# Kernel tuning notes

Hardware: AMD Instinct MI355X
Metric: run time of the kernel (lower is better)

The kernel has to match this reference:

```python
import jax, jax.numpy as jnp
import numpy as np


def _layernorm(x, g, b, eps=1e-5):
    mu = jnp.mean(x, axis=-1, keepdims=True)
    var = jnp.var(x, axis=-1, keepdims=True)
    return (x - mu) * jax.lax.rsqrt(var + eps) * g + b


def _forward(x_real, x_imag, dt, conv_w, conv_b, spec_re, spec_im, lam_re, lam_im,
             dt_param, sigma, noise_r, noise_i, ln_g, ln_b, W1, b1, w2, b2,
             Jg_W, Jg_b, Rg_W, Rg_b):
    B, T, C, H, W = x_real.shape
    x = x_real + 1j * x_imag  # complex field [B,T,C,H,W]

    # ---- spatial mixer: 3x3 conv applied to real/imag parts (linear op) ----
    def conv(z):
        z2 = z.reshape(B * T, C, H, W)
        y = jax.lax.conv_general_dilated(z2, conv_w, (1, 1), 'SAME',
                                         dimension_numbers=('NCHW', 'OIHW', 'NCHW'))
        return (y + conv_b[None, :, None, None]).reshape(B, T, C, H, W)
    x = x + (conv(x.real) + 1j * conv(x.imag))

    # ---- spectral mixer: pointwise complex filter in FFT domain ----
    Xf = jnp.fft.fft2(x, axes=(-2, -1), norm='ortho')
    filt = (spec_re + 1j * spec_im)[None, None]  # [1,1,C,H,W]
    x = x + jnp.fft.ifft2(Xf * filt, axes=(-2, -1), norm='ortho')

    # ---- metriplectic propagator: diagonal SSM scan in rfft2 space ----
    dt_eff = dt * jax.nn.softplus(dt_param)          # [C]
    dt_scalar = dt_eff.mean()
    xs = jnp.concatenate([x.real, x.imag], axis=0)   # [2B,T,C,H,W]; B_out=2B
    u = jnp.fft.rfft2(xs, axes=(-2, -1), norm='ortho')  # [2B,T,C,H,Wf]
    lam = -jax.nn.softplus(lam_re) + 1j * lam_im     # stable poles, [C]
    A = jnp.exp(lam * dt_eff.astype(jnp.complex64))  # [C]
    A = jnp.broadcast_to(A[None, None, :, None, None], u.shape)

    def comb(e1, e2):  # first-order linear recurrence h_t = a_t h_{t-1} + u_t
        a1, u1 = e1
        a2, u2 = e2
        return (a1 * a2, a2 * u1 + u2)
    _, h = jax.lax.associative_scan(comb, (A, u), axis=1)

    xt = jnp.fft.irfft2(h, s=(H, W), axes=(-2, -1), norm='ortho')  # [2B,T,C,H,W] real
    x_temporal = xt[:B] + 1j * xt[B:]

    noise = (noise_r + 1j * noise_i) * sigma * jnp.sqrt(dt_scalar)
    x = x + x_temporal + noise

    # ---- Port-Hamiltonian layer on real||imag channel concat ----
    xp = jnp.transpose(x, (0, 1, 3, 4, 2))                  # [B,T,H,W,C]
    xc = jnp.concatenate([xp.real, xp.imag], axis=-1)       # [B,T,H,W,2C]
    D = 2 * C
    x_in = _layernorm(xc, ln_g, ln_b)
    # grads of potential H = sum(MLP(x_in)) wrt x_in
    pot = lambda z: (jax.nn.silu(z @ W1 + b1) @ w2 + b2).sum()
    grads = jax.grad(pot)(x_in)
    M = (x_in @ Jg_W + Jg_b).reshape(*xc.shape[:-1], D, D)
    Jm = M - jnp.swapaxes(M, -1, -2)
    P = (x_in @ Rg_W + Rg_b).reshape(*xc.shape[:-1], D, D)
    R = jnp.einsum('...ki,...kj->...ij', P, P) + 1e-4 * jnp.eye(D, dtype=xc.dtype)
    update = jnp.einsum('...ij,...j->...i', Jm - R, grads)
    x_ph = xc + update * dt_scalar

    # output: [B,T,2C,H,W]; real half = out.real, imag half = out.imag
    return jnp.transpose(x_ph, (0, 1, 4, 2, 3))


def setup_inputs() -> dict:
    key = jax.random.key(0)
    ks = jax.random.split(key, 16)
    B, T, C, H, W = 2, 8, 16, 64, 64
    D = 2 * C
    hid = D * 4
    f32 = jnp.float32
    rn = lambda k, s, sc=1.0: jax.random.normal(k, s, f32) * sc
    return dict(
        x_real=rn(ks[0], (B, T, C, H, W)),
        x_imag=rn(ks[1], (B, T, C, H, W)),
        dt=jnp.asarray(0.1, f32),
        conv_w=rn(ks[2], (C, C, 3, 3), 0.05),
        conv_b=jnp.zeros((C,), f32),
        spec_re=rn(ks[3], (C, H, W), 0.1),
        spec_im=rn(ks[4], (C, H, W), 0.1),
        lam_re=rn(ks[5], (C,)),
        lam_im=rn(ks[6], (C,)),
        dt_param=rn(ks[7], (C,)),
        sigma=jnp.asarray(0.01, f32),
        noise_r=rn(ks[8], (B, T, C, H, W)),
        noise_i=rn(ks[9], (B, T, C, H, W)),
        ln_g=jnp.ones((D,), f32),
        ln_b=jnp.zeros((D,), f32),
        W1=rn(ks[10], (D, hid), 0.1),
        b1=jnp.zeros((hid,), f32),
        w2=rn(ks[11], (hid,), 0.1),
        b2=jnp.asarray(0.0, f32),
        Jg_W=rn(ks[12], (D, D * D), 0.02),
        Jg_b=jnp.zeros((D * D,), f32),
        Rg_W=rn(ks[13], (D, D * D), 0.02),
        Rg_b=jnp.zeros((D * D,), f32),
    )


def reference(x_real, x_imag, dt, conv_w, conv_b, spec_re, spec_im, lam_re, lam_im,
              dt_param, sigma, noise_r, noise_i, ln_g, ln_b, W1, b1, w2, b2,
              Jg_W, Jg_b, Rg_W, Rg_b):
    return _forward(x_real, x_imag, dt, conv_w, conv_b, spec_re, spec_im, lam_re,
                    lam_im, dt_param, sigma, noise_r, noise_i, ln_g, ln_b, W1, b1,
                    w2, b2, Jg_W, Jg_b, Rg_W, Rg_b)
```

## Files before the change

kernel.cpp:

```cpp
#include <hip/hip_runtime.h>
#include <math.h>
#include <utility>

#define Bb 2
#define Tt 8
#define Cc 16
#define Hh 64
#define Ww 64
#define Dd 32
#define HID 128
#define NPIX 4096
#define NIMG 256

typedef unsigned short ushort_t;
typedef unsigned int uint_t;
typedef __attribute__((ext_vector_type(8))) short short8;
typedef __attribute__((ext_vector_type(4))) float f32x4;
union U16 { uint4 u; short8 s; };

__device__ __forceinline__ float sp_f(float x) {
    return (x > 20.f) ? x : log1pf(expf(x));
}

__device__ __forceinline__ ushort_t f2bf(float f) {
    uint_t u = __float_as_uint(f);
    uint_t r = (u + 0x7fffu + ((u >> 16) & 1u)) >> 16;
    return (ushort_t)r;
}
__device__ __forceinline__ float bf2f(ushort_t h) { return __uint_as_float(((uint_t)h) << 16); }

__device__ __forceinline__ uint_t packbf(float hi, float lo) {
    return __builtin_amdgcn_perm(__float_as_uint(hi), __float_as_uint(lo), 0x07060302u);
}
__device__ __forceinline__ uint4 synth8(const float* gf, float xs) {
    uint4 r;
    r.x = packbf(gf[1] * xs, gf[0] * xs);
    r.y = packbf(gf[3] * xs, gf[2] * xs);
    r.z = packbf(gf[5] * xs, gf[4] * xs);
    r.w = packbf(gf[7] * xs, gf[6] * xs);
    return r;
}
__device__ __forceinline__ void expand8(uint4 v, float* f) {
    f[0] = __uint_as_float(v.x << 16); f[1] = __uint_as_float(v.x & 0xffff0000u);
    f[2] = __uint_as_float(v.y << 16); f[3] = __uint_as_float(v.y & 0xffff0000u);
    f[4] = __uint_as_float(v.z << 16); f[5] = __uint_as_float(v.z & 0xffff0000u);
    f[6] = __uint_as_float(v.w << 16); f[7] = __uint_as_float(v.w & 0xffff0000u);
}

template <typename F, int... Is>
__device__ __forceinline__ void unroll_impl(F&& f, std::integer_sequence<int, Is...>) {
    (f(std::integral_constant<int, Is>{}), ...);
}
template <int N, typename F>
__device__ __forceinline__ void cunroll(F&& f) {
    unroll_impl(f, std::make_integer_sequence<int, N>{});
}

#define MFMA16(a, b, c) __builtin_amdgcn_mfma_f32_16x16x32_bf16((a), (b), (c), 0, 0, 0)

struct cpx { float r, i; };
__device__ __forceinline__ cpx cadd(cpx a, cpx b) { return {a.r + b.r, a.i + b.i}; }
__device__ __forceinline__ cpx csub(cpx a, cpx b) { return {a.r - b.r, a.i - b.i}; }
__device__ __forceinline__ cpx cmulw(cpx a, float wr, float wi) {
    return {a.r * wr - a.i * wi, a.r * wi + a.i * wr};
}
template<int S>
__device__ __forceinline__ cpx cmulSi(cpx a) {
    return {-(float)S * a.i, (float)S * a.r};
}
template<int S>
__device__ __forceinline__ void dft8(cpx* y) {
    const float C = 0.70710678118654752f;
    cpx t0 = cadd(y[0], y[4]), t1 = csub(y[0], y[4]);
    cpx t2 = cadd(y[2], y[6]), t3 = csub(y[2], y[6]);
    cpx e0 = cadd(t0, t2), e2 = csub(t0, t2);
    cpx t3i = cmulSi<S>(t3);
    cpx e1 = cadd(t1, t3i), e3 = csub(t1, t3i);
    cpx u0 = cadd(y[1], y[5]), u1 = csub(y[1], y[5]);
    cpx u2 = cadd(y[3], y[7]), u3 = csub(y[3], y[7]);
    cpx o0 = cadd(u0, u2), o2 = csub(u0, u2);
    cpx u3i = cmulSi<S>(u3);
    cpx o1 = cadd(u1, u3i), o3 = csub(u1, u3i);
    o1 = cmulw(o1, C, (float)S * C);
    o2 = cmulSi<S>(o2);
    o3 = cmulw(o3, -C, (float)S * C);
    y[0] = cadd(e0, o0); y[4] = csub(e0, o0);
    y[1] = cadd(e1, o1); y[5] = csub(e1, o1);
    y[2] = cadd(e2, o2); y[6] = csub(e2, o2);
    y[3] = cadd(e3, o3); y[7] = csub(e3, o3);
}

template<int S>
__device__ __forceinline__ void fft2d_r8(float* reM, float* imM,
                                         const float* twr, const float* twi, int tid) {
    int j = tid & 63, g = tid >> 6;
    {
        cpx y[8];
        #pragma unroll
        for (int n1 = 0; n1 < 8; ++n1) {
            int a = j * 65 + n1 * 8 + g;
            y[n1] = {reM[a], imM[a]};
        }
        dft8<S>(y);
        #pragma unroll
        for (int k1 = 0; k1 < 8; ++k1) {
            int m = (g * k1) & 63;
            cpx b = cmulw(y[k1], twr[m], twi[m]);
            int a = j * 65 + k1 * 8 + g;
            reM[a] = b.r; imM[a] = b.i;
        }
    }
    __syncthreads();
    {
        cpx y[8];
        #pragma unroll
        for (int n2 = 0; n2 < 8; ++n2) {
            int a = j * 65 + g * 8 + n2;
            y[n2] = {reM[a], imM[a]};
        }
        dft8<S>(y);
        __syncthreads();
        #pragma unroll
        for (int k2 = 0; k2 < 8; ++k2) {
            int a = j * 65 + g + k2 * 8;
            reM[a] = y[k2].r; imM[a] = y[k2].i;
        }
    }
    __syncthreads();
    {
        cpx y[8];
        #pragma unroll
        for (int n1 = 0; n1 < 8; ++n1) {
            int a = (n1 * 8 + g) * 65 + j;
            y[n1] = {reM[a], imM[a]};
        }
        dft8<S>(y);
        #pragma unroll
        for (int k1 = 0; k1 < 8; ++k1) {
            int m = (g * k1) & 63;
            cpx b = cmulw(y[k1], twr[m], twi[m]);
            int a = (k1 * 8 + g) * 65 + j;
            reM[a] = b.r; imM[a] = b.i;
        }
    }
    __syncthreads();
    {
        cpx y[8];
        #pragma unroll
        for (int n2 = 0; n2 < 8; ++n2) {
            int a = (g * 8 + n2) * 65 + j;
            y[n2] = {reM[a], imM[a]};
        }
        dft8<S>(y);
        __syncthreads();
        #pragma unroll
        for (int k2 = 0; k2 < 8; ++k2) {
            int a = (g + k2 * 8) * 65 + j;
            reM[a] = y[k2].r; imM[a] = y[k2].i;
        }
    }
    __syncthreads();
}

__global__ __launch_bounds__(256)
void k_conv(const float* __restrict__ xr, const float* __restrict__ xi,
            const float* __restrict__ cw, const float* __restrict__ cb,
            float2* __restrict__ x1,
            const float* __restrict__ JW, const float* __restrict__ Jb,
            const float* __restrict__ RW, const float* __restrict__ Rb,
            const float* __restrict__ W1, const float* __restrict__ dtp,
            const float* __restrict__ dt_param,
            ushort_t* __restrict__ B1f, ushort_t* __restrict__ B2f,
            ushort_t* __restrict__ w1n, ushort_t* __restrict__ w1t,
            float* __restrict__ dts_out) {
    __shared__ float sre[Cc][18][18];
    __shared__ float sim[Cc][18][18];
    __shared__ float swt[8 * 16 * 12];
    __shared__ float sb[8];
    int tid = threadIdx.x;
    if (blockIdx.x >= 512) {
        const int N1 = 33 * 3072, N2 = 33 * 1024, N3 = 4096;
        int i = (blockIdx.x - 512) * 256 + tid;
        for (; i < N1 + N2 + N3; i += 40 * 256) {
            if (i < N1) {
                int s = i / 3072; int r = i % 3072;
                int ch = r >> 9; int lane = (r >> 3) & 63; int e = i & 7;
                int n = ch * 16 + (lane & 15);
                int k = s * 32 + ((lane >> 4) << 3) + e;
                float v;
                if (k < 1024) {
                    int d = k >> 5, rr = k & 31;
                    if (n < 32)      v = JW[d * 1024 + n * 32 + rr];
                    else if (n < 64) v = JW[d * 1024 + rr * 32 + (n - 32)];
                    else             v = RW[d * 1024 + (n - 64) * 32 + rr];
                } else {
                    int rr = k - 1024;
                    if (n < 32)      v = Jb[n * 32 + rr];
                    else if (n < 64) v = Jb[rr * 32 + (n - 32)];
                    else             v = Rb[(n - 64) * 32 + rr];
                }
                B1f[i] = f2bf(v);
            } else if (i < N1 + N2) {
                int i2 = i - N1;
                int s = i2 / 1024; int r = i2 % 1024;
                int ch = r >> 9; int lane = (r >> 3) & 63; int e = i2 & 7;
                int n = ch * 16 + (lane & 15);
                int k = s * 32 + ((lane >> 4) << 3) + e;
                float v;
                if (k < 1024) {
                    int d = k >> 5, kk = k & 31;
                    v = RW[d * 1024 + kk * 32 + n];
                } else {
                    v = Rb[(k - 1024) * 32 + n];
                }
                B2f[i2] = f2bf(v);
            } else {
                int i3 = i - N1 - N2;
                int d = i3 >> 7, h = i3 & 127;
                ushort_t v = f2bf(W1[i3]);
                w1n[i3] = v;
                w1t[h * 32 + d] = v;
            }
        }
        if (blockIdx.x == 512 && tid == 0) {
            float s = 0.f;
            for (int c = 0; c < Cc; ++c) s += sp_f(dt_param[c]);
            dts_out[0] = dtp[0] * s * (1.f / Cc);
        }
        return;
    }
    int blk = blockIdx.x;
    int bt = blk >> 5;
    int sub = blk & 31;
    int tile = sub >> 1, cohalf = sub & 1;
    int ty0 = (tile >> 2) * 16, tx0 = (tile & 3) * 16;
    for (int i = tid; i < 8 * 16 * 9; i += 256) {
        int g = i / 9, k = i % 9;
        swt[g * 12 + k] = cw[cohalf * 8 * 144 + i];
    }
    if (tid < 8) sb[tid] = cb[cohalf * 8 + tid];
    for (int i = tid; i < Cc * 18 * 18; i += 256) {
        int ci = i / 324; int r = i % 324; int y = r / 18, x = r % 18;
        int gy = ty0 + y - 1, gx = tx0 + x - 1;
        float vr = 0.f, vi = 0.f;
        if (gy >= 0 && gy < Hh && gx >= 0 && gx < Ww) {
            int gidx = (bt * Cc + ci) * NPIX + gy * Ww + gx;
            vr = xr[gidx]; vi = xi[gidx];
        }
        sre[ci][y][x] = vr; sim[ci][y][x] = vi;
    }
    __syncthreads();
    int py = tid >> 4, px = tid & 15;
    int gy = ty0 + py, gx = tx0 + px;
    float ar[8], ai[8];
    #pragma unroll
    for (int oc = 0; oc < 8; ++oc) {
        int cg = cohalf * 8 + oc;
        ar[oc] = sre[cg][py + 1][px + 1] + sb[oc];
        ai[oc] = sim[cg][py + 1][px + 1] + sb[oc];
    }
    for (int ci = 0; ci < Cc; ++ci) {
        float nr[9], ni[9];
        #pragma unroll
        for (int dy = 0; dy < 3; ++dy)
            #pragma unroll
            for (int dx = 0; dx < 3; ++dx) {
                nr[dy * 3 + dx] = sre[ci][py + dy][px + dx];
                ni[dy * 3 + dx] = sim[ci][py + dy][px + dx];
            }
        #pragma unroll
        for (int oc = 0; oc < 8; ++oc) {
            const float* wp = &swt[(oc * 16 + ci) * 12];
            float4 w0 = *(const float4*)&wp[0];
            float4 w1 = *(const float4*)&wp[4];
            float w8 = wp[8];
            ar[oc] += w0.x * nr[0] + w0.y * nr[1] + w0.z * nr[2]
                    + w0.w * nr[3] + w1.x * nr[4] + w1.y * nr[5]
                    + w1.z * nr[6] + w1.w * nr[7] + w8 * nr[8];
            ai[oc] += w0.x * ni[0] + w0.y * ni[1] + w0.z * ni[2]
                    + w0.w * ni[3] + w1.x * ni[4] + w1.y * ni[5]
                    + w1.z * ni[6] + w1.w * ni[7] + w8 * ni[8];
        }
    }
    #pragma unroll
    for (int oc = 0; oc < 8; ++oc)
        x1[(bt * Cc + cohalf * 8 + oc) * NPIX + gy * Ww + gx] = make_float2(ar[oc], ai[oc]);
}

__global__ __launch_bounds__(512)
void k_fft_fwd(const float2* __restrict__ x1,
               const float* __restrict__ spec_re, const float* __restrict__ spec_im,
               float2* __restrict__ X2f) {
    int img = blockIdx.x;
    int c = img % Cc;
    int tid = threadIdx.x;
    __shared__ float re[64 * 65], im[64 * 65];
    __shared__ float twr[64], twi[64];
    if (tid < 64) {
        float ang = -0.098174770424681038798f * (float)tid;
        twr[tid] = cosf(ang); twi[tid] = sinf(ang);
    }
    const float2* src = x1 + (size_t)img * NPIX;
    for (int idx = tid; idx < NPIX; idx += 512) {
        int h = idx >> 6, w = idx & 63;
        float2 v = src[idx];
        re[h * 65 + w] = v.x; im[h * 65 + w] = v.y;
    }
    __syncthreads();
    fft2d_r8<-1>(re, im, twr, twi, tid);
    const float* fr = spec_re + c * NPIX;
    const float* fi = spec_im + c * NPIX;
    float2* dst = X2f + (size_t)img * NPIX;
    for (int idx = tid; idx < NPIX; idx += 512) {
        int h = idx >> 6, w = idx & 63;
        float xr_ = re[h * 65 + w], xi_ = im[h * 65 + w];
        float gr = 1.f + fr[idx], gi = fi[idx];
        dst[idx] = make_float2(xr_ * gr - xi_ * gi, xi_ * gr + xr_ * gi);
    }
}

__global__ __launch_bounds__(256)
void k_scan2(const float2* __restrict__ Z,
             const float* __restrict__ lam_re, const float* __restrict__ lam_im,
             const float* __restrict__ dt_param, const float* __restrict__ dtp,
             float2* __restrict__ S) {
    int id = blockIdx.x * 256 + threadIdx.x;
    int w = id & 63;
    int c = (id >> 12) & 15;
    int b = id >> 16;
    float dte = dtp[0] * sp_f(dt_param[c]);
    float ea = expf(-sp_f(lam_re[c]) * dte);
    float ph = lam_im[c] * dte;
    float Ar = ea * cosf(ph), Ai = ea * sinf(ph);
    if (w > 32) Ai = -Ai;
    bool sc = (w == 0) || (w == 32);
    int pix = id & (NPIX - 1);
    int base = (b * Tt * Cc + c) * NPIX + pix;
    float s1r = 0.f, s1i = 0.f, s2r = 0.f, s2i = 0.f;
    #pragma unroll
    for (int t = 0; t < Tt; ++t) {
        int idx = base + t * (Cc * NPIX);
        float2 zv = Z[idx];
        float nr = Ar * s1r - Ai * s1i + zv.x;
        float ni = Ar * s1i + Ai * s1r + zv.y;
        s1r = nr; s1i = ni;
        float zr, zi;
        if (sc) {
            nr = Ar * s2r + Ai * s2i + zv.x;
            ni = Ar * s2i - Ai * s2r + zv.y;
            s2r = nr; s2i = ni;
            zr = 0.5f * (s1r + s2r); zi = 0.5f * (s1i + s2i);
        } else { zr = s1r; zi = s1i; }
        S[idx] = make_float2(zv.x + zr, zv.y + zi);
    }
}

__global__ __launch_bounds__(512)
void k_fft_inv(const float2* __restrict__ Sp,
               const float* __restrict__ noise_r, const float* __restrict__ noise_i,
               const float* __restrict__ sigma_p, const float* __restrict__ dts_p,
               float2* __restrict__ xf) {
    int img = blockIdx.x; int tid = threadIdx.x;
    __shared__ float re[64 * 65], im[64 * 65];
    __shared__ float twr[64], twi[64];
    if (tid < 64) {
        float ang = 0.098174770424681038798f * (float)tid;
        twr[tid] = cosf(ang); twi[tid] = sinf(ang);
    }
    const float2* src = Sp + (size_t)img * NPIX;
    for (int idx = tid; idx < NPIX; idx += 512) {
        int h = idx >> 6, w = idx & 63;
        float2 v = src[idx];
        re[h * 65 + w] = v.x; im[h * 65 + w] = v.y;
    }
    __syncthreads();
    fft2d_r8<1>(re, im, twr, twi, tid);
    float ns = sigma_p[0] * sqrtf(dts_p[0]);
    const float inv = 1.f / 4096.f;
    float2* dst = xf + (size_t)img * NPIX;
    const float* nr = noise_r + (size_t)img * NPIX;
    const float* ni = noise_i + (size_t)img * NPIX;
    for (int idx = tid; idx < NPIX; idx += 512) {
        int h = idx >> 6, w = idx & 63;
        dst[idx] = make_float2(re[h * 65 + w] * inv + ns * nr[idx],
                               im[h * 65 + w] * inv + ns * ni[idx]);
    }
}

__global__ __launch_bounds__(256, 2)
void k_ph(const float2* __restrict__ field,
          const float* __restrict__ ln_g, const float* __restrict__ ln_b,
          const float* __restrict__ b1, const float* __restrict__ w2,
          const ushort_t* __restrict__ w1n, const ushort_t* __restrict__ w1t,
          const ushort_t* __restrict__ B1f, const ushort_t* __restrict__ B2f,
          const float* __restrict__ dts_p,
          float* __restrict__ out) {
    __shared__ ushort_t xin_s[128 * 40];
    __shared__ ushort_t g_s[128 * 40];
    __shared__ ushort_t pg_s[128 * 40];
    __shared__ ushort_t A_s[128 * 136] __attribute__((aligned(16)));

    int tid = threadIdx.x;
    int bt = blockIdx.x >> 5;
    int pix0 = (blockIdx.x & 31) << 7;

    int p = tid & 127, half = tid >> 7;
    const float2* fbase = field + ((size_t)bt * 16) * NPIX + pix0 + p;
    float2 xv[8];
    float s1 = 0.f, s2 = 0.f;
    #pragma unroll
    for (int j = 0; j < 8; ++j) {
        xv[j] = fbase[(half * 8 + j) * NPIX];
        s1 += xv[j].x + xv[j].y;
        s2 += xv[j].x * xv[j].x + xv[j].y * xv[j].y;
    }
    float2* red = (float2*)A_s;
    red[p * 2 + half] = make_float2(s1, s2);
    __syncthreads();
    float2 r0 = red[p * 2], r1 = red[p * 2 + 1];
    float mu = (r0.x + r1.x) * 0.03125f;
    float var = (r0.y + r1.y) * 0.03125f - mu * mu;
    float rs = rsqrtf(var + 1e-5f);
    #pragma unroll
    for (int j = 0; j < 8; ++j) {
        int cf = half * 8 + j;
        xin_s[p * 40 + cf]      = f2bf((xv[j].x - mu) * rs * ln_g[cf] + ln_b[cf]);
        xin_s[p * 40 + cf + 16] = f2bf((xv[j].y - mu) * rs * ln_g[cf + 16] + ln_b[cf + 16]);
    }
    __syncthreads();

    int lane = tid & 63, wv = tid >> 6;
    int quad = lane >> 4, l15 = lane & 15;
    const f32x4 zero4 = {0.f, 0.f, 0.f, 0.f};
    int m0 = wv * 32;

    f32x4 zacc[2][8];
    #pragma unroll
    for (int mt = 0; mt < 2; ++mt)
        #pragma unroll
        for (int nt = 0; nt < 8; ++nt) zacc[mt][nt] = zero4;
    U16 az[2];
    #pragma unroll
    for (int mt = 0; mt < 2; ++mt)
        az[mt].u = *(const uint4*)&xin_s[(m0 + mt * 16 + l15) * 40 + quad * 8];
    #pragma unroll
    for (int nt = 0; nt < 8; ++nt) {
        U16 bz;
        bz.u = *(const uint4*)&w1t[(nt * 16 + l15) * 32 + quad * 8];
        zacc[0][nt] = MFMA16(az[0].s, bz.s, zacc[0][nt]);
        zacc[1][nt] = MFMA16(az[1].s, bz.s, zacc[1][nt]);
    }
    #pragma unroll
    for (int nt = 0; nt < 8; ++nt) {
        int col = nt * 16 + l15;
        float b1v = b1[col], w2v = w2[col];
        #pragma unroll
        for (int mt = 0; mt < 2; ++mt) {
            #pragma unroll
            for (int r = 0; r < 4; ++r) {
                int row = m0 + mt * 16 + quad * 4 + r;
                float z = zacc[mt][nt][r] + b1v;
                float s = 1.f / (1.f + expf(-z));
                float t = s * (1.f + z * (1.f - s)) * w2v;
                A_s[row * 136 + col] = f2bf(t);
            }
        }
    }
    __syncthreads();

    f32x4 gacc[2][2];
    #pragma unroll
    for (int mt = 0; mt < 2; ++mt)
        #pragma unroll
        for (int nt = 0; nt < 2; ++nt) gacc[mt][nt] = zero4;
    #pragma unroll
    for (int q = 0; q < 4; ++q) {
        U16 ag[2];
        #pragma unroll
        for (int mt = 0; mt < 2; ++mt)
            ag[mt].u = *(const uint4*)&A_s[(m0 + mt * 16 + l15) * 136 + q * 32 + quad * 8];
        #pragma unroll
        for (int nt = 0; nt < 2; ++nt) {
            U16 bg;
            bg.u = *(const uint4*)&w1n[(nt * 16 + l15) * 128 + q * 32 + quad * 8];
            gacc[0][nt] = MFMA16(ag[0].s, bg.s, gacc[0][nt]);
            gacc[1][nt] = MFMA16(ag[1].s, bg.s, gacc[1][nt]);
        }
    }
    #pragma unroll
    for (int mt = 0; mt < 2; ++mt)
        #pragma unroll
        for (int nt = 0; nt < 2; ++nt)
            #pragma unroll
            for (int r = 0; r < 4; ++r)
                g_s[(m0 + mt * 16 + quad * 4 + r) * 40 + nt * 16 + l15] = f2bf(gacc[mt][nt][r]);
    __syncthreads();

    const ushort_t* xr0 = &xin_s[(m0 + l15) * 40];
    const ushort_t* xr1 = &xin_s[(m0 + 16 + l15) * 40];
    uint4 gvp0 = *(const uint4*)&g_s[(m0 + l15) * 40 + quad * 8];
    uint4 gvp1 = *(const uint4*)&g_s[(m0 + 16 + l15) * 40 + quad * 8];
    float gf0[8], gf1[8];
    expand8(gvp0, gf0);
    expand8(gvp1, gf1);
    const uint4* B1v = (const uint4*)B1f;
    const uint4* B2v = (const uint4*)B2f;

    uint4 br[2][6];
    #pragma unroll
    for (int pf = 0; pf < 2; ++pf)
        #pragma unroll
        for (int ch = 0; ch < 6; ++ch)
            br[pf][ch] = B1v[(pf * 6 + ch) * 64 + lane];
    f32x4 acc1[6][2];
    #pragma unroll
    for (int ch = 0; ch < 6; ++ch) { acc1[ch][0] = zero4; acc1[ch][1] = zero4; }
    cunroll<33>([&](auto Sc) {
        constexpr int s = Sc.value;
        constexpr int cur = s & 1;
        U16 a0, a1;
        if constexpr (s < 32) {
            float x0 = bf2f(xr0[s]);
            float x1 = bf2f(xr1[s]);
            a0.u = synth8(gf0, x0);
            a1.u = synth8(gf1, x1);
        } else {
            a0.u = gvp0; a1.u = gvp1;
        }
        #pragma unroll
        for (int ch = 0; ch < 6; ++ch) {
            U16 b; b.u = br[cur][ch];
            acc1[ch][0] = MFMA16(a0.s, b.s, acc1[ch][0]);
            acc1[ch][1] = MFMA16(a1.s, b.s, acc1[ch][1]);
        }
        if constexpr (s + 2 < 33) {
            #pragma unroll
            for (int ch = 0; ch < 6; ++ch)
                br[cur][ch] = B1v[((s + 2) * 6 + ch) * 64 + lane];
        }
    });
    #pragma unroll
    for (int mt = 0; mt < 2; ++mt)
        #pragma unroll
        for (int c2 = 0; c2 < 2; ++c2)
            #pragma unroll
            for (int r = 0; r < 4; ++r)
                pg_s[(m0 + mt * 16 + quad * 4 + r) * 40 + c2 * 16 + l15] =
                    f2bf(acc1[4 + c2][mt][r]);
    __syncthreads();

    uint4 pgp0 = *(const uint4*)&pg_s[(m0 + l15) * 40 + quad * 8];
    uint4 pgp1 = *(const uint4*)&pg_s[(m0 + 16 + l15) * 40 + quad * 8];
    float pgf0[8], pgf1[8];
    expand8(pgp0, pgf0);
    expand8(pgp1, pgf1);
    uint4 br2[2][2];
    #pragma unroll
    for (int pf = 0; pf < 2; ++pf) {
        br2[pf][0] = B2v[(pf * 2 + 0) * 64 + lane];
        br2[pf][1] = B2v[(pf * 2 + 1) * 64 + lane];
    }
    f32x4 acc2[2][2];
    acc2[0][0] = zero4; acc2[0][1] = zero4; acc2[1][0] = zero4; acc2[1][1] = zero4;
    cunroll<33>([&](auto Sc) {
        constexpr int s = Sc.value;
        constexpr int cur = s & 1;
        U16 a0, a1;
        if constexpr (s < 32) {
            float x0 = bf2f(xr0[s]);
            float x1 = bf2f(xr1[s]);
            a0.u = synth8(pgf0, x0);
            a1.u = synth8(pgf1, x1);
        } else {
            a0.u = pgp0; a1.u = pgp1;
        }
        #pragma unroll
        for (int ch = 0; ch < 2; ++ch) {
            U16 b; b.u = br2[cur][ch];
            acc2[ch][0] = MFMA16(a0.s, b.s, acc2[ch][0]);
            acc2[ch][1] = MFMA16(a1.s, b.s, acc2[ch][1]);
        }
        if constexpr (s + 2 < 33) {
            br2[cur][0] = B2v[((s + 2) * 2 + 0) * 64 + lane];
            br2[cur][1] = B2v[((s + 2) * 2 + 1) * 64 + lane];
        }
    });

    __syncthreads();
    float* upd = (float*)A_s;
    #pragma unroll
    for (int mt = 0; mt < 2; ++mt) {
        #pragma unroll
        for (int c2 = 0; c2 < 2; ++c2) {
            int col = c2 * 16 + l15;
            #pragma unroll
            for (int r = 0; r < 4; ++r) {
                int row = m0 + mt * 16 + quad * 4 + r;
                float gval = bf2f(g_s[row * 40 + col]);
                upd[row * 33 + col] = (acc1[c2][mt][r] - acc1[c2 + 2][mt][r])
                                      - acc2[c2][mt][r] - 1e-4f * gval;
            }
        }
    }
    __syncthreads();
    float dts = dts_p[0];
    #pragma unroll
    for (int cc = 0; cc < 16; ++cc) {
        int c = half * 16 + cc;
        float2 v = fbase[cc * NPIX];
        float xcv = half ? v.y : v.x;
        out[((size_t)bt * 32 + c) * NPIX + pix0 + p] = xcv + dts * upd[p * 33 + c];
    }
}

extern "C" void kernel_launch(void* const* d_in, const int* in_sizes, int n_in,
                              void* d_out, int out_size, void* d_ws, size_t ws_size,
                              hipStream_t stream) {
    const float* x_real   = (const float*)d_in[0];
    const float* x_imag   = (const float*)d_in[1];
    const float* dt       = (const float*)d_in[2];
    const float* conv_w   = (const float*)d_in[3];
    const float* conv_b   = (const float*)d_in[4];
    const float* spec_re  = (const float*)d_in[5];
    const float* spec_im  = (const float*)d_in[6];
    const float* lam_re   = (const float*)d_in[7];
    const float* lam_im   = (const float*)d_in[8];
    const float* dt_param = (const float*)d_in[9];
    const float* sigma    = (const float*)d_in[10];
    const float* noise_r  = (const float*)d_in[11];
    const float* noise_i  = (const float*)d_in[12];
    const float* ln_g     = (const float*)d_in[13];
    const float* ln_b     = (const float*)d_in[14];
    const float* W1       = (const float*)d_in[15];
    const float* b1       = (const float*)d_in[16];
    const float* w2       = (const float*)d_in[17];
    const float* Jg_W     = (const float*)d_in[19];
    const float* Jg_b     = (const float*)d_in[20];
    const float* Rg_W     = (const float*)d_in[21];
    const float* Rg_b     = (const float*)d_in[22];

    float2* wsA = (float2*)d_ws;
    float2* wsB = wsA + 1048576;
    float2* wsS = wsB + 1048576;

    ushort_t* B1f = (ushort_t*)(wsS + 1048576);
    ushort_t* B2f = B1f + 33 * 3072;
    ushort_t* w1n = B2f + 33 * 1024;
    ushort_t* w1t = w1n + 4096;
    float*    dts = (float*)(w1t + 4096);

    k_conv<<<552, 256, 0, stream>>>(x_real, x_imag, conv_w, conv_b, wsA,
                                    Jg_W, Jg_b, Rg_W, Rg_b, W1, dt, dt_param,
                                    B1f, B2f, w1n, w1t, dts);
    k_fft_fwd<<<NIMG, 512, 0, stream>>>(wsA, spec_re, spec_im, wsB);
    k_scan2<<<512, 256, 0, stream>>>(wsB, lam_re, lam_im, dt_param, dt, wsS);
    k_fft_inv<<<NIMG, 512, 0, stream>>>(wsS, noise_r, noise_i, sigma, dts, wsA);
    k_ph<<<512, 256, 0, stream>>>(wsA, ln_g, ln_b, b1, w2, w1n, w1t, B1f, B2f, dts,
                                  (float*)d_out);
}
```

Measured before the change: 189.4 us.

## Fold J minus J-transpose into packed weights and give each PH wave 64 rows

The J and J-transpose weight blocks are pre-subtracted when the bf16 B1 operand is packed, so the first PH GEMM needs 4 output chunks instead of 6 and the later subtraction goes away. k_ph now runs 128-thread blocks, with each wave owning 64 pixel rows and a private LDS slice. This removes every block-level __syncthreads, reuses each B fragment across 4 M-tiles, and uses triple-buffered B prefetch. The cost is fewer waves per block and more accumulator registers per wave, which may limit latency hiding. Folding the subtraction before bf16 rounding also changes rounding slightly.

```diff
diff --git a/kernel.cpp b/kernel.cpp
--- a/kernel.cpp
+++ b/kernel.cpp
@@ -179,25 +179,23 @@
     __shared__ float sb[8];
     int tid = threadIdx.x;
     if (blockIdx.x >= 512) {
-        const int N1 = 33 * 3072, N2 = 33 * 1024, N3 = 4096;
+        const int N1 = 33 * 2048, N2 = 33 * 1024, N3 = 4096;
         int i = (blockIdx.x - 512) * 256 + tid;
         for (; i < N1 + N2 + N3; i += 40 * 256) {
             if (i < N1) {
-                int s = i / 3072; int r = i % 3072;
+                int s = i / 2048; int r = i % 2048;
                 int ch = r >> 9; int lane = (r >> 3) & 63; int e = i & 7;
                 int n = ch * 16 + (lane & 15);
                 int k = s * 32 + ((lane >> 4) << 3) + e;
                 float v;
                 if (k < 1024) {
                     int d = k >> 5, rr = k & 31;
-                    if (n < 32)      v = JW[d * 1024 + n * 32 + rr];
-                    else if (n < 64) v = JW[d * 1024 + rr * 32 + (n - 32)];
-                    else             v = RW[d * 1024 + (n - 64) * 32 + rr];
+                    if (n < 32) v = JW[d * 1024 + n * 32 + rr] - JW[d * 1024 + rr * 32 + n];
+                    else        v = RW[d * 1024 + (n - 32) * 32 + rr];
                 } else {
                     int rr = k - 1024;
-                    if (n < 32)      v = Jb[n * 32 + rr];
-                    else if (n < 64) v = Jb[rr * 32 + (n - 32)];
-                    else             v = Rb[(n - 64) * 32 + rr];
+                    if (n < 32) v = Jb[n * 32 + rr] - Jb[rr * 32 + n];
+                    else        v = Rb[(n - 32) * 32 + rr];
                 }
                 B1f[i] = f2bf(v);
             } else if (i < N1 + N2) {
@@ -387,7 +385,7 @@
     }
 }
 
-__global__ __launch_bounds__(256, 2)
+__global__ __launch_bounds__(128, 1)
 void k_ph(const float2* __restrict__ field,
           const float* __restrict__ ln_g, const float* __restrict__ ln_b,
           const float* __restrict__ b1, const float* __restrict__ w2,
@@ -397,219 +395,225 @@
           float* __restrict__ out) {
     __shared__ ushort_t xin_s[128 * 40];
     __shared__ ushort_t g_s[128 * 40];
-    __shared__ ushort_t pg_s[128 * 40];
-    __shared__ ushort_t A_s[128 * 136] __attribute__((aligned(16)));
-
+    __shared__ ushort_t A_st[2 * 4352];
     int tid = threadIdx.x;
     int bt = blockIdx.x >> 5;
     int pix0 = (blockIdx.x & 31) << 7;
-
-    int p = tid & 127, half = tid >> 7;
-    const float2* fbase = field + ((size_t)bt * 16) * NPIX + pix0 + p;
-    float2 xv[8];
-    float s1 = 0.f, s2 = 0.f;
-    #pragma unroll
-    for (int j = 0; j < 8; ++j) {
-        xv[j] = fbase[(half * 8 + j) * NPIX];
-        s1 += xv[j].x + xv[j].y;
-        s2 += xv[j].x * xv[j].x + xv[j].y * xv[j].y;
-    }
-    float2* red = (float2*)A_s;
-    red[p * 2 + half] = make_float2(s1, s2);
-    __syncthreads();
-    float2 r0 = red[p * 2], r1 = red[p * 2 + 1];
-    float mu = (r0.x + r1.x) * 0.03125f;
-    float var = (r0.y + r1.y) * 0.03125f - mu * mu;
-    float rs = rsqrtf(var + 1e-5f);
-    #pragma unroll
-    for (int j = 0; j < 8; ++j) {
-        int cf = half * 8 + j;
-        xin_s[p * 40 + cf]      = f2bf((xv[j].x - mu) * rs * ln_g[cf] + ln_b[cf]);
-        xin_s[p * 40 + cf + 16] = f2bf((xv[j].y - mu) * rs * ln_g[cf + 16] + ln_b[cf + 16]);
-    }
-    __syncthreads();
-
+    int p = tid;
     int lane = tid & 63, wv = tid >> 6;
     int quad = lane >> 4, l15 = lane & 15;
+    int m0 = wv * 64;
+    ushort_t* slice = &A_st[wv * 4352];
     const f32x4 zero4 = {0.f, 0.f, 0.f, 0.f};
-    int m0 = wv * 32;
-
-    f32x4 zacc[2][8];
-    #pragma unroll
-    for (int mt = 0; mt < 2; ++mt)
-        #pragma unroll
-        for (int nt = 0; nt < 8; ++nt) zacc[mt][nt] = zero4;
-    U16 az[2];
-    #pragma unroll
-    for (int mt = 0; mt < 2; ++mt)
-        az[mt].u = *(const uint4*)&xin_s[(m0 + mt * 16 + l15) * 40 + quad * 8];
-    #pragma unroll
-    for (int nt = 0; nt < 8; ++nt) {
-        U16 bz;
-        bz.u = *(const uint4*)&w1t[(nt * 16 + l15) * 32 + quad * 8];
-        zacc[0][nt] = MFMA16(az[0].s, bz.s, zacc[0][nt]);
-        zacc[1][nt] = MFMA16(az[1].s, bz.s, zacc[1][nt]);
-    }
-    #pragma unroll
-    for (int nt = 0; nt < 8; ++nt) {
-        int col = nt * 16 + l15;
-        float b1v = b1[col], w2v = w2[col];
-        #pragma unroll
-        for (int mt = 0; mt < 2; ++mt) {
-            #pragma unroll
-            for (int r = 0; r < 4; ++r) {
-                int row = m0 + mt * 16 + quad * 4 + r;
-                float z = zacc[mt][nt][r] + b1v;
-                float s = 1.f / (1.f + expf(-z));
-                float t = s * (1.f + z * (1.f - s)) * w2v;
-                A_s[row * 136 + col] = f2bf(t);
+
+    const float2* fbase = field + ((size_t)bt * 16) * NPIX + pix0 + p;
+    {
+        float2 xv[16];
+        float s1 = 0.f, s2 = 0.f;
+        #pragma unroll
+        for (int j = 0; j < 16; ++j) {
+            xv[j] = fbase[j * NPIX];
+            s1 += xv[j].x + xv[j].y;
+            s2 += xv[j].x * xv[j].x + xv[j].y * xv[j].y;
+        }
+        float mu = s1 * 0.03125f;
+        float var = s2 * 0.03125f - mu * mu;
+        float rs = rsqrtf(var + 1e-5f);
+        #pragma unroll
+        for (int j = 0; j < 16; ++j) {
+            xin_s[p * 40 + j]      = f2bf((xv[j].x - mu) * rs * ln_g[j] + ln_b[j]);
+            xin_s[p * 40 + 16 + j] = f2bf((xv[j].y - mu) * rs * ln_g[16 + j] + ln_b[16 + j]);
+        }
+    }
+
+    #pragma unroll
+    for (int hh = 0; hh < 2; ++hh) {
+        int hb = m0 + hh * 32;
+        U16 az[2];
+        #pragma unroll
+        for (int mt2 = 0; mt2 < 2; ++mt2)
+            az[mt2].u = *(const uint4*)&xin_s[(hb + mt2 * 16 + l15) * 40 + quad * 8];
+        f32x4 zacc[2][8];
+        #pragma unroll
+        for (int mt2 = 0; mt2 < 2; ++mt2)
+            #pragma unroll
+            for (int nt = 0; nt < 8; ++nt) zacc[mt2][nt] = zero4;
+        #pragma unroll
+        for (int nt = 0; nt < 8; ++nt) {
+            U16 bz;
+            bz.u = *(const uint4*)&w1t[(nt * 16 + l15) * 32 + quad * 8];
+            zacc[0][nt] = MFMA16(az[0].s, bz.s, zacc[0][nt]);
+            zacc[1][nt] = MFMA16(az[1].s, bz.s, zacc[1][nt]);
+        }
+        #pragma unroll
+        for (int nt = 0; nt < 8; ++nt) {
+            int col = nt * 16 + l15;
+            float b1v = b1[col], w2v = w2[col];
+            #pragma unroll
+            for (int mt2 = 0; mt2 < 2; ++mt2) {
+                #pragma unroll
+                for (int r = 0; r < 4; ++r) {
+                    int lrow = mt2 * 16 + quad * 4 + r;
+                    float z = zacc[mt2][nt][r] + b1v;
+                    float s = 1.f / (1.f + expf(-z));
+                    float t = s * (1.f + z * (1.f - s)) * w2v;
+                    slice[lrow * 136 + col] = f2bf(t);
+                }
             }
         }
-    }
-    __syncthreads();
-
-    f32x4 gacc[2][2];
-    #pragma unroll
-    for (int mt = 0; mt < 2; ++mt)
-        #pragma unroll
-        for (int nt = 0; nt < 2; ++nt) gacc[mt][nt] = zero4;
-    #pragma unroll
-    for (int q = 0; q < 4; ++q) {
-        U16 ag[2];
-        #pragma unroll
-        for (int mt = 0; mt < 2; ++mt)
-            ag[mt].u = *(const uint4*)&A_s[(m0 + mt * 16 + l15) * 136 + q * 32 + quad * 8];
-        #pragma unroll
-        for (int nt = 0; nt < 2; ++nt) {
-            U16 bg;
-            bg.u = *(const uint4*)&w1n[(nt * 16 + l15) * 128 + q * 32 + quad * 8];
-            gacc[0][nt] = MFMA16(ag[0].s, bg.s, gacc[0][nt]);
-            gacc[1][nt] = MFMA16(ag[1].s, bg.s, gacc[1][nt]);
-        }
-    }
-    #pragma unroll
-    for (int mt = 0; mt < 2; ++mt)
-        #pragma unroll
-        for (int nt = 0; nt < 2; ++nt)
-            #pragma unroll
-            for (int r = 0; r < 4; ++r)
-                g_s[(m0 + mt * 16 + quad * 4 + r) * 40 + nt * 16 + l15] = f2bf(gacc[mt][nt][r]);
-    __syncthreads();
-
-    const ushort_t* xr0 = &xin_s[(m0 + l15) * 40];
-    const ushort_t* xr1 = &xin_s[(m0 + 16 + l15) * 40];
-    uint4 gvp0 = *(const uint4*)&g_s[(m0 + l15) * 40 + quad * 8];
-    uint4 gvp1 = *(const uint4*)&g_s[(m0 + 16 + l15) * 40 + quad * 8];
-    float gf0[8], gf1[8];
-    expand8(gvp0, gf0);
-    expand8(gvp1, gf1);
+        f32x4 gacc[2][2];
+        gacc[0][0] = zero4; gacc[0][1] = zero4; gacc[1][0] = zero4; gacc[1][1] = zero4;
+        #pragma unroll
+        for (int q = 0; q < 4; ++q) {
+            U16 ag[2];
+            #pragma unroll
+            for (int mt2 = 0; mt2 < 2; ++mt2)
+                ag[mt2].u = *(const uint4*)&slice[(mt2 * 16 + l15) * 136 + q * 32 + quad * 8];
+            #pragma unroll
+            for (int nt2 = 0; nt2 < 2; ++nt2) {
+                U16 bg;
+                bg.u = *(const uint4*)&w1n[(nt2 * 16 + l15) * 128 + q * 32 + quad * 8];
+                gacc[0][nt2] = MFMA16(ag[0].s, bg.s, gacc[0][nt2]);
+                gacc[1][nt2] = MFMA16(ag[1].s, bg.s, gacc[1][nt2]);
+            }
+        }
+        #pragma unroll
+        for (int mt2 = 0; mt2 < 2; ++mt2)
+            #pragma unroll
+            for (int nt2 = 0; nt2 < 2; ++nt2)
+                #pragma unroll
+                for (int r = 0; r < 4; ++r)
+                    g_s[(hb + mt2 * 16 + quad * 4 + r) * 40 + nt2 * 16 + l15] =
+                        f2bf(gacc[mt2][nt2][r]);
+    }
+
+    const ushort_t* xr[4];
+    uint4 gvp[4];
+    float gf[4][8];
+    #pragma unroll
+    for (int mt = 0; mt < 4; ++mt) {
+        int row = m0 + mt * 16 + l15;
+        xr[mt] = &xin_s[row * 40];
+        gvp[mt] = *(const uint4*)&g_s[row * 40 + quad * 8];
+        expand8(gvp[mt], gf[mt]);
+    }
     const uint4* B1v = (const uint4*)B1f;
     const uint4* B2v = (const uint4*)B2f;
 
-    uint4 br[2][6];
-    #pragma unroll
-    for (int pf = 0; pf < 2; ++pf)
-        #pragma unroll
-        for (int ch = 0; ch < 6; ++ch)
-            br[pf][ch] = B1v[(pf * 6 + ch) * 64 + lane];
-    f32x4 acc1[6][2];
-    #pragma unroll
-    for (int ch = 0; ch < 6; ++ch) { acc1[ch][0] = zero4; acc1[ch][1] = zero4; }
+    uint4 br[3][4];
+    #pragma unroll
+    for (int pf = 0; pf < 3; ++pf)
+        #pragma unroll
+        for (int ch = 0; ch < 4; ++ch)
+            br[pf][ch] = B1v[(pf * 4 + ch) * 64 + lane];
+    f32x4 acc1[4][4];
+    #pragma unroll
+    for (int ch = 0; ch < 4; ++ch)
+        #pragma unroll
+        for (int mt = 0; mt < 4; ++mt) acc1[ch][mt] = zero4;
     cunroll<33>([&](auto Sc) {
         constexpr int s = Sc.value;
-        constexpr int cur = s & 1;
-        U16 a0, a1;
+        constexpr int slot = s % 3;
+        U16 a[4];
         if constexpr (s < 32) {
-            float x0 = bf2f(xr0[s]);
-            float x1 = bf2f(xr1[s]);
-            a0.u = synth8(gf0, x0);
-            a1.u = synth8(gf1, x1);
+            #pragma unroll
+            for (int mt = 0; mt < 4; ++mt) {
+                float xs = bf2f(xr[mt][s]);
+                a[mt].u = synth8(gf[mt], xs);
+            }
         } else {
-            a0.u = gvp0; a1.u = gvp1;
-        }
-        #pragma unroll
-        for (int ch = 0; ch < 6; ++ch) {
-            U16 b; b.u = br[cur][ch];
-            acc1[ch][0] = MFMA16(a0.s, b.s, acc1[ch][0]);
-            acc1[ch][1] = MFMA16(a1.s, b.s, acc1[ch][1]);
-        }
-        if constexpr (s + 2 < 33) {
-            #pragma unroll
-            for (int ch = 0; ch < 6; ++ch)
-                br[cur][ch] = B1v[((s + 2) * 6 + ch) * 64 + lane];
+            #pragma unroll
+            for (int mt = 0; mt < 4; ++mt) a[mt].u = gvp[mt];
+        }
+        #pragma unroll
+        for (int ch = 0; ch < 4; ++ch) {
+            U16 b; b.u = br[slot][ch];
+            #pragma unroll
+            for (int mt = 0; mt < 4; ++mt)
+                acc1[ch][mt] = MFMA16(a[mt].s, b.s, acc1[ch][mt]);
+        }
+        if constexpr (s + 3 < 33) {
+            #pragma unroll
+            for (int ch = 0; ch < 4; ++ch)
+                br[slot][ch] = B1v[((s + 3) * 4 + ch) * 64 + lane];
         }
     });
     #pragma unroll
-    for (int mt = 0; mt < 2; ++mt)
+    for (int mt = 0; mt < 4; ++mt)
         #pragma unroll
         for (int c2 = 0; c2 < 2; ++c2)
             #pragma unroll
             for (int r = 0; r < 4; ++r)
-                pg_s[(m0 + mt * 16 + quad * 4 + r) * 40 + c2 * 16 + l15] =
-                    f2bf(acc1[4 + c2][mt][r]);
-    __syncthreads();
-
-    uint4 pgp0 = *(const uint4*)&pg_s[(m0 + l15) * 40 + quad * 8];
-    uint4 pgp1 = *(const uint4*)&pg_s[(m0 + 16 + l15) * 40 + quad * 8];
-    float pgf0[8], pgf1[8];
-    expand8(pgp0, pgf0);
-    expand8(pgp1, pgf1);
-    uint4 br2[2][2];
-    #pragma unroll
-    for (int pf = 0; pf < 2; ++pf) {
+                slice[(mt * 16 + quad * 4 + r) * 40 + c2 * 16 + l15] =
+                    f2bf(acc1[2 + c2][mt][r]);
+
+    uint4 pgp[4];
+    float pgf[4][8];
+    #pragma unroll
+    for (int mt = 0; mt < 4; ++mt) {
+        pgp[mt] = *(const uint4*)&slice[(mt * 16 + l15) * 40 + quad * 8];
+        expand8(pgp[mt], pgf[mt]);
+    }
+    uint4 br2[3][2];
+    #pragma unroll
+    for (int pf = 0; pf < 3; ++pf) {
         br2[pf][0] = B2v[(pf * 2 + 0) * 64 + lane];
         br2[pf][1] = B2v[(pf * 2 + 1) * 64 + lane];
     }
-    f32x4 acc2[2][2];
-    acc2[0][0] = zero4; acc2[0][1] = zero4; acc2[1][0] = zero4; acc2[1][1] = zero4;
+    f32x4 acc2[2][4];
+    #pragma unroll
+    for (int ch = 0; ch < 2; ++ch)
+        #pragma unroll
+        for (int mt = 0; mt < 4; ++mt) acc2[ch][mt] = zero4;
     cunroll<33>([&](auto Sc) {
         constexpr int s = Sc.value;
-        constexpr int cur = s & 1;
-        U16 a0, a1;
+        constexpr int slot = s % 3;
+        U16 a[4];
         if constexpr (s < 32) {
-            float x0 = bf2f(xr0[s]);
-            float x1 = bf2f(xr1[s]);
-            a0.u = synth8(pgf0, x0);
-            a1.u = synth8(pgf1, x1);
+            #pragma unroll
+            for (int mt = 0; mt < 4; ++mt) {
+                float xs = bf2f(xr[mt][s]);
+                a[mt].u = synth8(pgf[mt], xs);
+            }
         } else {
-            a0.u = pgp0; a1.u = pgp1;
+            #pragma unroll
+            for (int mt = 0; mt < 4; ++mt) a[mt].u = pgp[mt];
         }
         #pragma unroll
         for (int ch = 0; ch < 2; ++ch) {
-            U16 b; b.u = br2[cur][ch];
-            acc2[ch][0] = MFMA16(a0.s, b.s, acc2[ch][0]);
-            acc2[ch][1] = MFMA16(a1.s, b.s, acc2[ch][1]);
-        }
-        if constexpr (s + 2 < 33) {
-            br2[cur][0] = B2v[((s + 2) * 2 + 0) * 64 + lane];
-            br2[cur][1] = B2v[((s + 2) * 2 + 1) * 64 + lane];
+            U16 b; b.u = br2[slot][ch];
+            #pragma unroll
+            for (int mt = 0; mt < 4; ++mt)
+                acc2[ch][mt] = MFMA16(a[mt].s, b.s, acc2[ch][mt]);
+        }
+        if constexpr (s + 3 < 33) {
+            br2[slot][0] = B2v[((s + 3) * 2 + 0) * 64 + lane];
+            br2[slot][1] = B2v[((s + 3) * 2 + 1) * 64 + lane];
         }
     });
 
-    __syncthreads();
-    float* upd = (float*)A_s;
-    #pragma unroll
-    for (int mt = 0; mt < 2; ++mt) {
-        #pragma unroll
-        for (int c2 = 0; c2 < 2; ++c2) {
-            int col = c2 * 16 + l15;
+    float* updS = (float*)slice;
+    #pragma unroll
+    for (int c2 = 0; c2 < 2; ++c2) {
+        int col = c2 * 16 + l15;
+        #pragma unroll
+        for (int mt = 0; mt < 4; ++mt) {
             #pragma unroll
             for (int r = 0; r < 4; ++r) {
-                int row = m0 + mt * 16 + quad * 4 + r;
-                float gval = bf2f(g_s[row * 40 + col]);
-                upd[row * 33 + col] = (acc1[c2][mt][r] - acc1[c2 + 2][mt][r])
-                                      - acc2[c2][mt][r] - 1e-4f * gval;
+                int lrow = mt * 16 + quad * 4 + r;
+                float gval = bf2f(g_s[(m0 + lrow) * 40 + col]);
+                updS[lrow * 33 + col] = acc1[c2][mt][r] - acc2[c2][mt][r] - 1e-4f * gval;
             }
         }
     }
-    __syncthreads();
     float dts = dts_p[0];
+    const float* updR = (const float*)&A_st[wv * 4352];
+    int lr = tid & 63;
     #pragma unroll
     for (int cc = 0; cc < 16; ++cc) {
-        int c = half * 16 + cc;
         float2 v = fbase[cc * NPIX];
-        float xcv = half ? v.y : v.x;
-        out[((size_t)bt * 32 + c) * NPIX + pix0 + p] = xcv + dts * upd[p * 33 + c];
+        out[((size_t)bt * 32 + cc) * NPIX + pix0 + p] = v.x + dts * updR[lr * 33 + cc];
+        out[((size_t)bt * 32 + 16 + cc) * NPIX + pix0 + p] = v.y + dts * updR[lr * 33 + 16 + cc];
     }
 }
 
@@ -644,7 +648,7 @@
     float2* wsS = wsB + 1048576;
 
     ushort_t* B1f = (ushort_t*)(wsS + 1048576);
-    ushort_t* B2f = B1f + 33 * 3072;
+    ushort_t* B2f = B1f + 33 * 2048;
     ushort_t* w1n = B2f + 33 * 1024;
     ushort_t* w1t = w1n + 4096;
     float*    dts = (float*)(w1t + 4096);
@@ -655,6 +659,6 @@
     k_fft_fwd<<<NIMG, 512, 0, stream>>>(wsA, spec_re, spec_im, wsB);
     k_scan2<<<512, 256, 0, stream>>>(wsB, lam_re, lam_im, dt_param, dt, wsS);
     k_fft_inv<<<NIMG, 512, 0, stream>>>(wsS, noise_r, noise_i, sigma, dts, wsA);
-    k_ph<<<512, 256, 0, stream>>>(wsA, ln_g, ln_b, b1, w2, w1n, w1t, B1f, B2f, dts,
+    k_ph<<<512, 128, 0, stream>>>(wsA, ln_g, ln_b, b1, w2, w1n, w1t, B1f, B2f, dts,
                                   (float*)d_out);
 }
```

New measurement: 197.9 us. 1.05x slower.
